# Kernel optimization log

Hardware: AMD Instinct MI355X
Metric: run time of the kernel (lower is better)

Reference implementation:

```python
import jax, jax.numpy as jnp
import numpy as np

H = 16
DH = 64  # n_state // n_head = 1024 // 16
EPS = 1e-6


def phi(x):
    return jax.nn.silu(x) + 1.0


def setup_inputs() -> dict:
    key = jax.random.key(0)
    ks = jax.random.split(key, 9)
    B, C, Tq, Tk = 8, 1024, 1500, 1500
    s = 1.0 / np.sqrt(C).astype(np.float32)
    return {
        "x": jax.random.normal(ks[0], (B, C, Tq, 1), jnp.float32),
        "xa": jax.random.normal(ks[1], (B, C, Tk, 1), jnp.float32),
        "Wq": jax.random.normal(ks[2], (C, C), jnp.float32) * s,
        "bq": jax.random.normal(ks[3], (C,), jnp.float32) * s,
        "Wk": jax.random.normal(ks[4], (C, C), jnp.float32) * s,
        "Wv": jax.random.normal(ks[5], (C, C), jnp.float32) * s,
        "bv": jax.random.normal(ks[6], (C,), jnp.float32) * s,
        "Wo": jax.random.normal(ks[7], (C, C), jnp.float32) * s,
        "bo": jax.random.normal(ks[8], (C,), jnp.float32) * s,
    }


def reference(x, xa, Wq, bq, Wk, Wv, bv, Wo, bo):
    # x: (B,C,Tq,1), xa: (B,C,Tk,1). 1x1 conv2d == matmul over channel dim.
    xq = x[..., 0]   # (B,C,Tq)
    xk = xa[..., 0]  # (B,C,Tk)
    q = jnp.einsum('oc,bct->bot', Wq, xq) + bq[None, :, None]
    k = jnp.einsum('oc,bct->bot', Wk, xk)  # key has no bias
    v = jnp.einsum('oc,bct->bot', Wv, xk) + bv[None, :, None]

    B, C, Tq = q.shape
    Tk = k.shape[2]
    pq = phi(q).reshape(B, H, DH, Tq)
    pk = phi(k).reshape(B, H, DH, Tk)
    vv = v.reshape(B, H, DH, Tk)

    k_sum = pk.sum(axis=3)            # (B,H,Dh) : sum_t phi(k)
    kv_sum = (pk * vv).sum(axis=3)    # (B,H,Dh) : diagonal phi(k)*v sum (as in source)
    den = jnp.einsum('bhdt,bhd->bht', pq, k_sum) + EPS  # (B,H,Tq)

    out = pq * kv_sum[..., None] / den[:, :, None, :]   # (B,H,Dh,Tq)
    out = out.reshape(B, C, Tq) / jnp.sqrt(jnp.asarray(DH, out.dtype))
    y = jnp.einsum('oc,bct->bot', Wo, out) + bo[None, :, None]
    return y[..., None]  # (B,C,Tq,1)
```

## Files before the change

kernel.cpp:

```cpp
#include <hip/hip_runtime.h>

typedef __attribute__((ext_vector_type(4))) float  f32x4;
typedef __attribute__((ext_vector_type(4))) float  float4v;
typedef __attribute__((ext_vector_type(8))) short  short8;
typedef __attribute__((ext_vector_type(4))) short  short4v;

#define TQ 1500
#define TP 1536
#define CC 1024
#define EPS 1e-6f

#define XT_OFF    ((size_t)0)
#define XAT_OFF   ((size_t)25165824)
#define OUT_OFF   ((size_t)50331648)
#define WB_OFF    ((size_t)75497472)
#define KSUM_OFF  ((size_t)83886080)
#define KVSUM_OFF ((size_t)83918848)

#define VMCNT4() asm volatile("s_waitcnt vmcnt(4)" ::: "memory")
#define VMCNT2() asm volatile("s_waitcnt vmcnt(2)" ::: "memory")
#define VMCNT0() asm volatile("s_waitcnt vmcnt(0)" ::: "memory")
#define LGKM0()  asm volatile("s_waitcnt lgkmcnt(0)" ::: "memory")
#define SBAR()   __builtin_amdgcn_s_barrier()
#define SCHED0() __builtin_amdgcn_sched_barrier(0)

__device__ __forceinline__ float bf2f(short s) {
    union { unsigned u; float f; } v; v.u = ((unsigned)(unsigned short)s) << 16; return v.f;
}
__device__ __forceinline__ short f2bf(float f) {
    union { float f; unsigned u; } v; v.f = f;
    unsigned r = (v.u + 0x7FFFu + ((v.u >> 16) & 1u)) >> 16;
    return (short)r;
}
__device__ __forceinline__ float phi_f(float x) {
    return x / (1.f + __expf(-x)) + 1.f;
}
__device__ __forceinline__ void gl_lds16(const void* g, void* l) {
    __builtin_amdgcn_global_load_lds((const __attribute__((address_space(1))) void*)g,
                                     (__attribute__((address_space(3))) void*)l, 16, 0, 0);
}


__global__ __launch_bounds__(256)
void conv_w_kernel(const float* __restrict__ w0, const float* __restrict__ w1,
                   const float* __restrict__ w2, const float* __restrict__ w3,
                   short* __restrict__ o0, short* __restrict__ o1,
                   short* __restrict__ o2, short* __restrict__ o3)
{
    const int i = (blockIdx.x * 256 + threadIdx.x) * 4;
    float4v a = *(const float4v*)(w0 + i);
    float4v b = *(const float4v*)(w1 + i);
    float4v c = *(const float4v*)(w2 + i);
    float4v d = *(const float4v*)(w3 + i);
    short4v ra, rb, rc, rd;
#pragma unroll
    for (int j = 0; j < 4; ++j) {
        ra[j] = f2bf(a[j]); rb[j] = f2bf(b[j]); rc[j] = f2bf(c[j]); rd[j] = f2bf(d[j]);
    }
    *(short4v*)(o0 + i) = ra;
    *(short4v*)(o1 + i) = rb;
    *(short4v*)(o2 + i) = rc;
    *(short4v*)(o3 + i) = rd;
}

__global__ __launch_bounds__(256)
void xpose_kernel(const float* __restrict__ x, const float* __restrict__ xa,
                  short* __restrict__ xT, short* __restrict__ xaT)
{
    __shared__ float tile[64][65];
    const int z  = blockIdx.z;
    const int b  = z & 7;
    const float* src = (z < 8) ? x : xa;
    short* dst       = (z < 8) ? xT : xaT;
    const int c0 = blockIdx.y * 64;
    const int t0 = blockIdx.x * 64;
    const int tl = threadIdx.x & 63;
    const int q  = threadIdx.x >> 6;
    const int t  = t0 + tl;
#pragma unroll
    for (int i = 0; i < 16; ++i) {
        const int cl = q * 16 + i;
        float v = 0.f;
        if (t < TQ) v = src[((size_t)b * CC + c0 + cl) * TQ + t];
        tile[cl][tl] = v;
    }
    __syncthreads();
#pragma unroll
    for (int i = 0; i < 16; ++i) {
        const int t2 = q * 16 + i;
        dst[((size_t)b * TP + t0 + t2) * CC + c0 + tl] = f2bf(tile[tl][t2]);
    }
}


__global__ __launch_bounds__(512, 4)
void gemm_q_out_kernel(const short* __restrict__ xT, const short* __restrict__ Wqb,
                       const float* __restrict__ bq, const float* __restrict__ ksum,
                       const float* __restrict__ kvsum, short* __restrict__ outT)
{
    __shared__ short lds[4][8192];
    const int f    = blockIdx.x;
    const int L    = (f & 7) * 96 + (f >> 3);
    const int nt   = L % 8;
    const int mrow = L / 8;
    const int b    = mrow / 12;
    const int tid  = threadIdx.x;
    const int wave = tid >> 6, lane = tid & 63;
    const int wr = wave >> 1;
    const int wc = wave & 1;
    const int rl = lane & 15;
    const int q4 = lane >> 4;
    const int rg = (q4 ^ ((rl >> 1) & 3)) << 3;
    const int rgrp = q4;

    const int srow = tid >> 2;
    const int skc  = ((tid & 3) ^ ((srow >> 1) & 3)) << 3;
    const short* aSrc = xT  + (size_t)(mrow * 128 + srow) * CC + skc;
    const short* bSrc = Wqb + (size_t)(nt   * 128 + srow) * CC + skc;
    const int dstOff = wave * 512;

    const int aoff0 = (wr * 32 + rl) * 32 + rg;
    const int boff0 = 4096 + (wc * 64 + rl) * 32 + rg;

    f32x4 acc[2][4] = {};

#pragma unroll
    for (int k0 = 0; k0 < 3; ++k0) {
        gl_lds16(aSrc + k0 * 32, &lds[k0][dstOff]);
        gl_lds16(bSrc + k0 * 32, &lds[k0][4096 + dstOff]);
    }
    VMCNT4(); SBAR();

#pragma unroll 1
    for (int kt = 0; kt < 32; ++kt) {
        if (kt < 29) {
            const int pn = (kt + 3) & 3;
            gl_lds16(aSrc + (kt + 3) * 32, &lds[pn][dstOff]);
            gl_lds16(bSrc + (kt + 3) * 32, &lds[pn][4096 + dstOff]);
        }
        const int p = kt & 3;
        const short* ba = &lds[p][aoff0];
        const short* bb = &lds[p][boff0];
        short8 ra[2], rb[4];
        ra[0] = *(const short8*)(ba);
        ra[1] = *(const short8*)(ba + 512);
        rb[0] = *(const short8*)(bb);
        rb[1] = *(const short8*)(bb + 512);
        rb[2] = *(const short8*)(bb + 1024);
        rb[3] = *(const short8*)(bb + 1536);
        LGKM0(); SCHED0();
        __builtin_amdgcn_s_setprio(1);
#pragma unroll
        for (int i = 0; i < 2; ++i)
#pragma unroll
            for (int j = 0; j < 4; ++j)
                acc[i][j] = __builtin_amdgcn_mfma_f32_16x16x32_bf16(ra[i], rb[j], acc[i][j], 0, 0, 0);
        __builtin_amdgcn_s_setprio(0);
        if (kt < 29)       { VMCNT4(); }
        else if (kt == 29) { VMCNT2(); }
        else if (kt == 30) { VMCNT0(); }
        if (kt < 31) SBAR();
    }

    float bias[4], ks[4], kv[4];
#pragma unroll
    for (int j = 0; j < 4; ++j) {
        const int c = nt * 128 + wc * 64 + j * 16 + rl;
        bias[j] = bq[c];
        ks[j]   = ksum[b * CC + c];
        kv[j]   = kvsum[b * CC + c];
    }
#pragma unroll
    for (int i = 0; i < 2; ++i)
#pragma unroll
        for (int j = 0; j < 4; ++j)
#pragma unroll
            for (int r = 0; r < 4; ++r)
                acc[i][j][r] = phi_f(acc[i][j][r] + bias[j]);
#pragma unroll
    for (int i = 0; i < 2; ++i) {
#pragma unroll
        for (int r = 0; r < 4; ++r) {
            float d = acc[i][0][r] * ks[0] + acc[i][1][r] * ks[1]
                    + acc[i][2][r] * ks[2] + acc[i][3][r] * ks[3];
            d += __shfl_xor(d, 1); d += __shfl_xor(d, 2);
            d += __shfl_xor(d, 4); d += __shfl_xor(d, 8);
            const float inv = 0.125f / (d + EPS);
            const int trow = mrow * 128 + wr * 32 + i * 16 + rgrp * 4 + r;
#pragma unroll
            for (int j = 0; j < 4; ++j) {
                const int c = nt * 128 + wc * 64 + j * 16 + rl;
                outT[(size_t)trow * CC + c] = f2bf(acc[i][j][r] * kv[j] * inv);
            }
        }
    }
}

__global__ __launch_bounds__(512, 4)
void gemm_kv_kernel(const short* __restrict__ xaT, const short* __restrict__ Wkb,
                    const short* __restrict__ Wvb, const float* __restrict__ bv,
                    float* __restrict__ ksum, float* __restrict__ kvsum)
{
    __shared__ short lds[4][8192];
    const int f    = blockIdx.x;
    const int L    = (f & 7) * 192 + (f >> 3);
    const int cb   = L % 16;
    const int mrow = L / 16;
    const int b    = mrow / 12;
    const int tid  = threadIdx.x;
    const int wave = tid >> 6, lane = tid & 63;
    const int wr = wave >> 1;
    const int wc = wave & 1;
    const int rl = lane & 15;
    const int q4 = lane >> 4;
    const int rg = (q4 ^ ((rl >> 1) & 3)) << 3;
    const int rgrp = q4;

    const int srow = tid >> 2;
    const int skc  = ((tid & 3) ^ ((srow >> 1) & 3)) << 3;
    const short* aSrc = xaT + (size_t)(mrow * 128 + srow) * CC + skc;
    const short* bSrc = (srow < 64)
        ? Wkb + (size_t)(cb * 64 + srow) * CC + skc
        : Wvb + (size_t)(cb * 64 + srow - 64) * CC + skc;
    const int dstOff = wave * 512;

    const int aoff0 = (wr * 32 + rl) * 32 + rg;
    const int boffK = 4096 + (wc * 32 + rl) * 32 + rg;
    const int boffV = boffK + 2048;

    f32x4 acc[2][4] = {};

#pragma unroll
    for (int k0 = 0; k0 < 3; ++k0) {
        gl_lds16(aSrc + k0 * 32, &lds[k0][dstOff]);
        gl_lds16(bSrc + k0 * 32, &lds[k0][4096 + dstOff]);
    }
    VMCNT4(); SBAR();

#pragma unroll 1
    for (int kt = 0; kt < 32; ++kt) {
        if (kt < 29) {
            const int pn = (kt + 3) & 3;
            gl_lds16(aSrc + (kt + 3) * 32, &lds[pn][dstOff]);
            gl_lds16(bSrc + (kt + 3) * 32, &lds[pn][4096 + dstOff]);
        }
        const int p = kt & 3;
        const short* ba = &lds[p][aoff0];
        short8 ra[2], rb[4];
        ra[0] = *(const short8*)(ba);
        ra[1] = *(const short8*)(ba + 512);
        rb[0] = *(const short8*)(&lds[p][boffK]);
        rb[1] = *(const short8*)(&lds[p][boffK + 512]);
        rb[2] = *(const short8*)(&lds[p][boffV]);
        rb[3] = *(const short8*)(&lds[p][boffV + 512]);
        LGKM0(); SCHED0();
        __builtin_amdgcn_s_setprio(1);
#pragma unroll
        for (int i = 0; i < 2; ++i)
#pragma unroll
            for (int j = 0; j < 4; ++j)
                acc[i][j] = __builtin_amdgcn_mfma_f32_16x16x32_bf16(ra[i], rb[j], acc[i][j], 0, 0, 0);
        __builtin_amdgcn_s_setprio(0);
        if (kt < 29)       { VMCNT4(); }
        else if (kt == 29) { VMCNT2(); }
        else if (kt == 30) { VMCNT0(); }
        if (kt < 31) SBAR();
    }

    const int tbase = (mrow % 12) * 128 + wr * 32 + rgrp * 4;
#pragma unroll
    for (int jj = 0; jj < 2; ++jj) {
        const int c = cb * 64 + wc * 32 + jj * 16 + rl;
        const float bvc = bv[c];
        float sk = 0.f, skv = 0.f;
#pragma unroll
        for (int i = 0; i < 2; ++i) {
#pragma unroll
            for (int r = 0; r < 4; ++r) {
                if (tbase + i * 16 + r < TQ) {
                    float pk = phi_f(acc[i][jj][r]);
                    float vv = acc[i][jj + 2][r] + bvc;
                    sk  += pk;
                    skv += pk * vv;
                }
            }
        }
        sk  += __shfl_xor(sk, 16);  sk  += __shfl_xor(sk, 32);
        skv += __shfl_xor(skv, 16); skv += __shfl_xor(skv, 32);
        if (rgrp == 0) {
            atomicAdd(&ksum[b * CC + c], sk);
            atomicAdd(&kvsum[b * CC + c], skv);
        }
    }
}

__global__ __launch_bounds__(512, 4)
void gemm_o_kernel(const short* __restrict__ Wob, const short* __restrict__ outT,
                   const float* __restrict__ bo, float* __restrict__ y)
{
    __shared__ short lds[4][8192];
    const int f    = blockIdx.x;
    const int L    = (f & 7) * 96 + (f >> 3);
    const int ct   = L % 8;
    const int rest = L / 8;
    const int b    = rest / 12;
    const int tt   = rest % 12;
    const int tid  = threadIdx.x;
    const int wave = tid >> 6, lane = tid & 63;
    const int wr = wave >> 1;
    const int wc = wave & 1;
    const int rl = lane & 15;
    const int q4 = lane >> 4;
    const int rg = (q4 ^ ((rl >> 1) & 3)) << 3;
    const int rgrp = q4;

    const int srow = tid >> 2;
    const int skc  = ((tid & 3) ^ ((srow >> 1) & 3)) << 3;
    const short* aSrc = Wob  + (size_t)(ct * 128 + srow) * CC + skc;
    const short* bSrc = outT + (size_t)(rest * 128 + srow) * CC + skc;
    const int dstOff = wave * 512;

    const int aoff0 = (wr * 32 + rl) * 32 + rg;
    const int boff0 = 4096 + (wc * 64 + rl) * 32 + rg;

    f32x4 acc[2][4] = {};

#pragma unroll
    for (int k0 = 0; k0 < 3; ++k0) {
        gl_lds16(aSrc + k0 * 32, &lds[k0][dstOff]);
        gl_lds16(bSrc + k0 * 32, &lds[k0][4096 + dstOff]);
    }
    VMCNT4(); SBAR();

#pragma unroll 1
    for (int kt = 0; kt < 32; ++kt) {
        if (kt < 29) {
            const int pn = (kt + 3) & 3;
            gl_lds16(aSrc + (kt + 3) * 32, &lds[pn][dstOff]);
            gl_lds16(bSrc + (kt + 3) * 32, &lds[pn][4096 + dstOff]);
        }
        const int p = kt & 3;
        const short* ba = &lds[p][aoff0];
        const short* bb = &lds[p][boff0];
        short8 ra[2], rb[4];
        ra[0] = *(const short8*)(ba);
        ra[1] = *(const short8*)(ba + 512);
        rb[0] = *(const short8*)(bb);
        rb[1] = *(const short8*)(bb + 512);
        rb[2] = *(const short8*)(bb + 1024);
        rb[3] = *(const short8*)(bb + 1536);
        LGKM0(); SCHED0();
        __builtin_amdgcn_s_setprio(1);
#pragma unroll
        for (int i = 0; i < 2; ++i)
#pragma unroll
            for (int j = 0; j < 4; ++j)
                acc[i][j] = __builtin_amdgcn_mfma_f32_16x16x32_bf16(ra[i], rb[j], acc[i][j], 0, 0, 0);
        __builtin_amdgcn_s_setprio(0);
        if (kt < 29)       { VMCNT4(); }
        else if (kt == 29) { VMCNT2(); }
        else if (kt == 30) { VMCNT0(); }
        if (kt < 31) SBAR();
    }

#pragma unroll
    for (int j = 0; j < 4; ++j) {
        const int t = tt * 128 + wc * 64 + j * 16 + rl;
        if (t >= TQ) continue;
#pragma unroll
        for (int i = 0; i < 2; ++i) {
            const int cbase = ct * 128 + wr * 32 + i * 16 + rgrp * 4;
#pragma unroll
            for (int r = 0; r < 4; ++r) {
                const int c = cbase + r;
                y[((size_t)b * CC + c) * TQ + t] = acc[i][j][r] + bo[c];
            }
        }
    }
}

extern "C" void kernel_launch(void* const* d_in, const int* in_sizes, int n_in,
                              void* d_out, int out_size, void* d_ws, size_t ws_size,
                              hipStream_t stream)
{
    (void)in_sizes; (void)n_in; (void)out_size; (void)ws_size;
    const float* x  = (const float*)d_in[0];
    const float* xa = (const float*)d_in[1];
    const float* Wq = (const float*)d_in[2];
    const float* bq = (const float*)d_in[3];
    const float* Wk = (const float*)d_in[4];
    const float* Wv = (const float*)d_in[5];
    const float* bv = (const float*)d_in[6];
    const float* Wo = (const float*)d_in[7];
    const float* bo = (const float*)d_in[8];
    float* y = (float*)d_out;
    char* ws = (char*)d_ws;

    short* xT    = (short*)(ws + XT_OFF);
    short* xaT   = (short*)(ws + XAT_OFF);
    short* outT  = (short*)(ws + OUT_OFF);
    short* Wqb   = (short*)(ws + WB_OFF);
    short* Wkb   = Wqb + (size_t)CC * CC;
    short* Wvb   = Wkb + (size_t)CC * CC;
    short* Wob   = Wvb + (size_t)CC * CC;
    float* ksum  = (float*)(ws + KSUM_OFF);
    float* kvsum = (float*)(ws + KVSUM_OFF);

    conv_w_kernel<<<dim3(CC * CC / 4 / 256), 256, 0, stream>>>(Wq, Wk, Wv, Wo, Wqb, Wkb, Wvb, Wob);
    xpose_kernel<<<dim3(TP / 64, CC / 64, 16), 256, 0, stream>>>(x, xa, xT, xaT);
    hipMemsetAsync(ws + KSUM_OFF, 0, 65536, stream);

    gemm_kv_kernel<<<dim3(1536), 512, 0, stream>>>(xaT, Wkb, Wvb, bv, ksum, kvsum);
    gemm_q_out_kernel<<<dim3(768), 512, 0, stream>>>(xT, Wqb, bq, ksum, kvsum, outT);
    gemm_o_kernel<<<dim3(768), 512, 0, stream>>>(Wob, outT, bo, y);
}
```

Baseline: 321.3 us.

## Use 4-wave blocks with 64x64 warp tiles and 3-stage LDS ring in GEMMs

All three GEMM kernels go from 8 waves per 128x128 tile to 4 waves, each wave now computing a 64x64 sub-tile (4x4 MFMA accumulators instead of 2x4). This doubles per-wave register reuse of LDS fragments and halves LDS reads per MFMA. The LDS ring shrinks from 4 to 3 stages, with prefetch distance 2, which reduces LDS footprint and so can raise occupancy. The costs are more accumulator registers per thread, fewer waves to hide latency, and a shallower prefetch pipeline.

```diff
diff --git a/kernel.cpp b/kernel.cpp
--- a/kernel.cpp
+++ b/kernel.cpp
@@ -18,7 +18,6 @@
 #define KVSUM_OFF ((size_t)83918848)
 
 #define VMCNT4() asm volatile("s_waitcnt vmcnt(4)" ::: "memory")
-#define VMCNT2() asm volatile("s_waitcnt vmcnt(2)" ::: "memory")
 #define VMCNT0() asm volatile("s_waitcnt vmcnt(0)" ::: "memory")
 #define LGKM0()  asm volatile("s_waitcnt lgkmcnt(0)" ::: "memory")
 #define SBAR()   __builtin_amdgcn_s_barrier()
@@ -93,12 +92,12 @@
 }
 
 
-__global__ __launch_bounds__(512, 4)
+__global__ __launch_bounds__(256, 4)
 void gemm_q_out_kernel(const short* __restrict__ xT, const short* __restrict__ Wqb,
                        const float* __restrict__ bq, const float* __restrict__ ksum,
                        const float* __restrict__ kvsum, short* __restrict__ outT)
 {
-    __shared__ short lds[4][8192];
+    __shared__ short lds[3][8192];
     const int f    = blockIdx.x;
     const int L    = (f & 7) * 96 + (f >> 3);
     const int nt   = L % 8;
@@ -111,55 +110,57 @@
     const int rl = lane & 15;
     const int q4 = lane >> 4;
     const int rg = (q4 ^ ((rl >> 1) & 3)) << 3;
-    const int rgrp = q4;
-
-    const int srow = tid >> 2;
-    const int skc  = ((tid & 3) ^ ((srow >> 1) & 3)) << 3;
-    const short* aSrc = xT  + (size_t)(mrow * 128 + srow) * CC + skc;
-    const short* bSrc = Wqb + (size_t)(nt   * 128 + srow) * CC + skc;
-    const int dstOff = wave * 512;
-
-    const int aoff0 = (wr * 32 + rl) * 32 + rg;
+
+    const int lrow = lane >> 2;
+    const int kc   = ((lane & 3) ^ ((lrow >> 1) & 3)) << 3;
+    const int row0 = wave * 32 + lrow;
+    const short* aP0 = xT  + (size_t)(mrow * 128 + row0) * CC + kc;
+    const short* aP1 = aP0 + 16 * CC;
+    const short* bP0 = Wqb + (size_t)(nt * 128 + row0) * CC + kc;
+    const short* bP1 = bP0 + 16 * CC;
+    const int aD0 = wave * 1024, aD1 = aD0 + 512;
+    const int bD0 = 4096 + aD0,  bD1 = bD0 + 512;
+
+    const int aoff0 = (wr * 64 + rl) * 32 + rg;
     const int boff0 = 4096 + (wc * 64 + rl) * 32 + rg;
 
-    f32x4 acc[2][4] = {};
-
-#pragma unroll
-    for (int k0 = 0; k0 < 3; ++k0) {
-        gl_lds16(aSrc + k0 * 32, &lds[k0][dstOff]);
-        gl_lds16(bSrc + k0 * 32, &lds[k0][4096 + dstOff]);
+    f32x4 acc[4][4] = {};
+
+#pragma unroll
+    for (int s = 0; s < 2; ++s) {
+        gl_lds16(aP0, &lds[s][aD0]); gl_lds16(aP1, &lds[s][aD1]);
+        gl_lds16(bP0, &lds[s][bD0]); gl_lds16(bP1, &lds[s][bD1]);
+        aP0 += 32; aP1 += 32; bP0 += 32; bP1 += 32;
     }
     VMCNT4(); SBAR();
 
+    int cur = 0;
 #pragma unroll 1
     for (int kt = 0; kt < 32; ++kt) {
-        if (kt < 29) {
-            const int pn = (kt + 3) & 3;
-            gl_lds16(aSrc + (kt + 3) * 32, &lds[pn][dstOff]);
-            gl_lds16(bSrc + (kt + 3) * 32, &lds[pn][4096 + dstOff]);
-        }
-        const int p = kt & 3;
-        const short* ba = &lds[p][aoff0];
-        const short* bb = &lds[p][boff0];
-        short8 ra[2], rb[4];
-        ra[0] = *(const short8*)(ba);
-        ra[1] = *(const short8*)(ba + 512);
-        rb[0] = *(const short8*)(bb);
-        rb[1] = *(const short8*)(bb + 512);
-        rb[2] = *(const short8*)(bb + 1024);
-        rb[3] = *(const short8*)(bb + 1536);
+        if (kt <= 29) {
+            const int pn = (cur == 0) ? 2 : cur - 1;
+            gl_lds16(aP0, &lds[pn][aD0]); gl_lds16(aP1, &lds[pn][aD1]);
+            gl_lds16(bP0, &lds[pn][bD0]); gl_lds16(bP1, &lds[pn][bD1]);
+            aP0 += 32; aP1 += 32; bP0 += 32; bP1 += 32;
+        }
+        short8 ra[4], rb[4];
+#pragma unroll
+        for (int i = 0; i < 4; ++i) {
+            ra[i] = *(const short8*)&lds[cur][aoff0 + i * 512];
+            rb[i] = *(const short8*)&lds[cur][boff0 + i * 512];
+        }
         LGKM0(); SCHED0();
         __builtin_amdgcn_s_setprio(1);
 #pragma unroll
-        for (int i = 0; i < 2; ++i)
+        for (int i = 0; i < 4; ++i)
 #pragma unroll
             for (int j = 0; j < 4; ++j)
                 acc[i][j] = __builtin_amdgcn_mfma_f32_16x16x32_bf16(ra[i], rb[j], acc[i][j], 0, 0, 0);
         __builtin_amdgcn_s_setprio(0);
-        if (kt < 29)       { VMCNT4(); }
-        else if (kt == 29) { VMCNT2(); }
+        if (kt <= 29)      { VMCNT4(); }
         else if (kt == 30) { VMCNT0(); }
         if (kt < 31) SBAR();
+        cur = (cur == 2) ? 0 : cur + 1;
     }
 
     float bias[4], ks[4], kv[4];
@@ -171,14 +172,14 @@
         kv[j]   = kvsum[b * CC + c];
     }
 #pragma unroll
-    for (int i = 0; i < 2; ++i)
+    for (int i = 0; i < 4; ++i)
 #pragma unroll
         for (int j = 0; j < 4; ++j)
 #pragma unroll
             for (int r = 0; r < 4; ++r)
                 acc[i][j][r] = phi_f(acc[i][j][r] + bias[j]);
 #pragma unroll
-    for (int i = 0; i < 2; ++i) {
+    for (int i = 0; i < 4; ++i) {
 #pragma unroll
         for (int r = 0; r < 4; ++r) {
             float d = acc[i][0][r] * ks[0] + acc[i][1][r] * ks[1]
@@ -186,7 +187,7 @@
             d += __shfl_xor(d, 1); d += __shfl_xor(d, 2);
             d += __shfl_xor(d, 4); d += __shfl_xor(d, 8);
             const float inv = 0.125f / (d + EPS);
-            const int trow = mrow * 128 + wr * 32 + i * 16 + rgrp * 4 + r;
+            const int trow = mrow * 128 + wr * 64 + i * 16 + q4 * 4 + r;
 #pragma unroll
             for (int j = 0; j < 4; ++j) {
                 const int c = nt * 128 + wc * 64 + j * 16 + rl;
@@ -196,12 +197,12 @@
     }
 }
 
-__global__ __launch_bounds__(512, 4)
+__global__ __launch_bounds__(256, 4)
 void gemm_kv_kernel(const short* __restrict__ xaT, const short* __restrict__ Wkb,
                     const short* __restrict__ Wvb, const float* __restrict__ bv,
                     float* __restrict__ ksum, float* __restrict__ kvsum)
 {
-    __shared__ short lds[4][8192];
+    __shared__ short lds[3][8192];
     const int f    = blockIdx.x;
     const int L    = (f & 7) * 192 + (f >> 3);
     const int cb   = L % 16;
@@ -214,70 +215,77 @@
     const int rl = lane & 15;
     const int q4 = lane >> 4;
     const int rg = (q4 ^ ((rl >> 1) & 3)) << 3;
-    const int rgrp = q4;
-
-    const int srow = tid >> 2;
-    const int skc  = ((tid & 3) ^ ((srow >> 1) & 3)) << 3;
-    const short* aSrc = xaT + (size_t)(mrow * 128 + srow) * CC + skc;
-    const short* bSrc = (srow < 64)
-        ? Wkb + (size_t)(cb * 64 + srow) * CC + skc
-        : Wvb + (size_t)(cb * 64 + srow - 64) * CC + skc;
-    const int dstOff = wave * 512;
-
-    const int aoff0 = (wr * 32 + rl) * 32 + rg;
+
+    const int lrow = lane >> 2;
+    const int kc   = ((lane & 3) ^ ((lrow >> 1) & 3)) << 3;
+    const int row0 = wave * 32 + lrow;
+    const short* aP0 = xaT + (size_t)(mrow * 128 + row0) * CC + kc;
+    const short* aP1 = aP0 + 16 * CC;
+    const short* bPanel = (wave < 2)
+        ? Wkb + (size_t)cb * 64 * CC
+        : Wvb + (size_t)cb * 64 * CC - (size_t)64 * CC;
+    const short* bP0 = bPanel + (size_t)row0 * CC + kc;
+    const short* bP1 = bP0 + 16 * CC;
+    const int aD0 = wave * 1024, aD1 = aD0 + 512;
+    const int bD0 = 4096 + aD0,  bD1 = bD0 + 512;
+
+    const int aoff0 = (wr * 64 + rl) * 32 + rg;
     const int boffK = 4096 + (wc * 32 + rl) * 32 + rg;
     const int boffV = boffK + 2048;
 
-    f32x4 acc[2][4] = {};
-
-#pragma unroll
-    for (int k0 = 0; k0 < 3; ++k0) {
-        gl_lds16(aSrc + k0 * 32, &lds[k0][dstOff]);
-        gl_lds16(bSrc + k0 * 32, &lds[k0][4096 + dstOff]);
+    f32x4 acc[4][4] = {};
+
+#pragma unroll
+    for (int s = 0; s < 2; ++s) {
+        gl_lds16(aP0, &lds[s][aD0]); gl_lds16(aP1, &lds[s][aD1]);
+        gl_lds16(bP0, &lds[s][bD0]); gl_lds16(bP1, &lds[s][bD1]);
+        aP0 += 32; aP1 += 32; bP0 += 32; bP1 += 32;
     }
     VMCNT4(); SBAR();
 
+    int cur = 0;
 #pragma unroll 1
     for (int kt = 0; kt < 32; ++kt) {
-        if (kt < 29) {
-            const int pn = (kt + 3) & 3;
-            gl_lds16(aSrc + (kt + 3) * 32, &lds[pn][dstOff]);
-            gl_lds16(bSrc + (kt + 3) * 32, &lds[pn][4096 + dstOff]);
-        }
-        const int p = kt & 3;
-        const short* ba = &lds[p][aoff0];
-        short8 ra[2], rb[4];
-        ra[0] = *(const short8*)(ba);
-        ra[1] = *(const short8*)(ba + 512);
-        rb[0] = *(const short8*)(&lds[p][boffK]);
-        rb[1] = *(const short8*)(&lds[p][boffK + 512]);
-        rb[2] = *(const short8*)(&lds[p][boffV]);
-        rb[3] = *(const short8*)(&lds[p][boffV + 512]);
+        if (kt <= 29) {
+            const int pn = (cur == 0) ? 2 : cur - 1;
+            gl_lds16(aP0, &lds[pn][aD0]); gl_lds16(aP1, &lds[pn][aD1]);
+            gl_lds16(bP0, &lds[pn][bD0]); gl_lds16(bP1, &lds[pn][bD1]);
+            aP0 += 32; aP1 += 32; bP0 += 32; bP1 += 32;
+        }
+        short8 ra[4], rb[4];
+#pragma unroll
+        for (int i = 0; i < 4; ++i)
+            ra[i] = *(const short8*)&lds[cur][aoff0 + i * 512];
+#pragma unroll
+        for (int j = 0; j < 2; ++j) {
+            rb[j]     = *(const short8*)&lds[cur][boffK + j * 512];
+            rb[j + 2] = *(const short8*)&lds[cur][boffV + j * 512];
+        }
         LGKM0(); SCHED0();
         __builtin_amdgcn_s_setprio(1);
 #pragma unroll
-        for (int i = 0; i < 2; ++i)
+        for (int i = 0; i < 4; ++i)
 #pragma unroll
             for (int j = 0; j < 4; ++j)
                 acc[i][j] = __builtin_amdgcn_mfma_f32_16x16x32_bf16(ra[i], rb[j], acc[i][j], 0, 0, 0);
         __builtin_amdgcn_s_setprio(0);
-        if (kt < 29)       { VMCNT4(); }
-        else if (kt == 29) { VMCNT2(); }
+        if (kt <= 29)      { VMCNT4(); }
         else if (kt == 30) { VMCNT0(); }
         if (kt < 31) SBAR();
-    }
-
-    const int tbase = (mrow % 12) * 128 + wr * 32 + rgrp * 4;
+        cur = (cur == 2) ? 0 : cur + 1;
+    }
+
+    const int tq0 = (mrow % 12) * 128 + wr * 64 + q4 * 4;
 #pragma unroll
     for (int jj = 0; jj < 2; ++jj) {
         const int c = cb * 64 + wc * 32 + jj * 16 + rl;
         const float bvc = bv[c];
         float sk = 0.f, skv = 0.f;
 #pragma unroll
-        for (int i = 0; i < 2; ++i) {
+        for (int i = 0; i < 4; ++i) {
 #pragma unroll
             for (int r = 0; r < 4; ++r) {
-                if (tbase + i * 16 + r < TQ) {
+                if (tq0 + i * 16 + r < TQ) {
                     float pk = phi_f(acc[i][jj][r]);
                     float vv = acc[i][jj + 2][r] + bvc;
                     sk  += pk;
@@ -287,18 +295,18 @@
         }
         sk  += __shfl_xor(sk, 16);  sk  += __shfl_xor(sk, 32);
         skv += __shfl_xor(skv, 16); skv += __shfl_xor(skv, 32);
-        if (rgrp == 0) {
+        if (q4 == 0) {
             atomicAdd(&ksum[b * CC + c], sk);
             atomicAdd(&kvsum[b * CC + c], skv);
         }
     }
 }
 
-__global__ __launch_bounds__(512, 4)
+__global__ __launch_bounds__(256, 4)
 void gemm_o_kernel(const short* __restrict__ Wob, const short* __restrict__ outT,
                    const float* __restrict__ bo, float* __restrict__ y)
 {
-    __shared__ short lds[4][8192];
+    __shared__ short lds[3][8192];
     const int f    = blockIdx.x;
     const int L    = (f & 7) * 96 + (f >> 3);
     const int ct   = L % 8;
@@ -312,55 +320,57 @@
     const int rl = lane & 15;
     const int q4 = lane >> 4;
     const int rg = (q4 ^ ((rl >> 1) & 3)) << 3;
-    const int rgrp = q4;
-
-    const int srow = tid >> 2;
-    const int skc  = ((tid & 3) ^ ((srow >> 1) & 3)) << 3;
-    const short* aSrc = Wob  + (size_t)(ct * 128 + srow) * CC + skc;
-    const short* bSrc = outT + (size_t)(rest * 128 + srow) * CC + skc;
-    const int dstOff = wave * 512;
-
-    const int aoff0 = (wr * 32 + rl) * 32 + rg;
+
+    const int lrow = lane >> 2;
+    const int kc   = ((lane & 3) ^ ((lrow >> 1) & 3)) << 3;
+    const int row0 = wave * 32 + lrow;
+    const short* aP0 = Wob  + (size_t)(ct * 128 + row0) * CC + kc;
+    const short* aP1 = aP0 + 16 * CC;
+    const short* bP0 = outT + (size_t)(rest * 128 + row0) * CC + kc;
+    const short* bP1 = bP0 + 16 * CC;
+    const int aD0 = wave * 1024, aD1 = aD0 + 512;
+    const int bD0 = 4096 + aD0,  bD1 = bD0 + 512;
+
+    const int aoff0 = (wr * 64 + rl) * 32 + rg;
     const int boff0 = 4096 + (wc * 64 + rl) * 32 + rg;
 
-    f32x4 acc[2][4] = {};
-
-#pragma unroll
-    for (int k0 = 0; k0 < 3; ++k0) {
-        gl_lds16(aSrc + k0 * 32, &lds[k0][dstOff]);
-        gl_lds16(bSrc + k0 * 32, &lds[k0][4096 + dstOff]);
+    f32x4 acc[4][4] = {};
+
+#pragma unroll
+    for (int s = 0; s < 2; ++s) {
+        gl_lds16(aP0, &lds[s][aD0]); gl_lds16(aP1, &lds[s][aD1]);
+        gl_lds16(bP0, &lds[s][bD0]); gl_lds16(bP1, &lds[s][bD1]);
+        aP0 += 32; aP1 += 32; bP0 += 32; bP1 += 32;
     }
     VMCNT4(); SBAR();
 
+    int cur = 0;
 #pragma unroll 1
     for (int kt = 0; kt < 32; ++kt) {
-        if (kt < 29) {
-            const int pn = (kt + 3) & 3;
-            gl_lds16(aSrc + (kt + 3) * 32, &lds[pn][dstOff]);
-            gl_lds16(bSrc + (kt + 3) * 32, &lds[pn][4096 + dstOff]);
-        }
-        const int p = kt & 3;
-        const short* ba = &lds[p][aoff0];
-        const short* bb = &lds[p][boff0];
-        short8 ra[2], rb[4];
-        ra[0] = *(const short8*)(ba);
-        ra[1] = *(const short8*)(ba + 512);
-        rb[0] = *(const short8*)(bb);
-        rb[1] = *(const short8*)(bb + 512);
-        rb[2] = *(const short8*)(bb + 1024);
-        rb[3] = *(const short8*)(bb + 1536);
+        if (kt <= 29) {
+            const int pn = (cur == 0) ? 2 : cur - 1;
+            gl_lds16(aP0, &lds[pn][aD0]); gl_lds16(aP1, &lds[pn][aD1]);
+            gl_lds16(bP0, &lds[pn][bD0]); gl_lds16(bP1, &lds[pn][bD1]);
+            aP0 += 32; aP1 += 32; bP0 += 32; bP1 += 32;
+        }
+        short8 ra[4], rb[4];
+#pragma unroll
+        for (int i = 0; i < 4; ++i) {
+            ra[i] = *(const short8*)&lds[cur][aoff0 + i * 512];
+            rb[i] = *(const short8*)&lds[cur][boff0 + i * 512];
+        }
         LGKM0(); SCHED0();
         __builtin_amdgcn_s_setprio(1);
 #pragma unroll
-        for (int i = 0; i < 2; ++i)
+        for (int i = 0; i < 4; ++i)
 #pragma unroll
             for (int j = 0; j < 4; ++j)
                 acc[i][j] = __builtin_amdgcn_mfma_f32_16x16x32_bf16(ra[i], rb[j], acc[i][j], 0, 0, 0);
         __builtin_amdgcn_s_setprio(0);
-        if (kt < 29)       { VMCNT4(); }
-        else if (kt == 29) { VMCNT2(); }
+        if (kt <= 29)      { VMCNT4(); }
         else if (kt == 30) { VMCNT0(); }
         if (kt < 31) SBAR();
+        cur = (cur == 2) ? 0 : cur + 1;
     }
 
 #pragma unroll
@@ -368,8 +378,8 @@
         const int t = tt * 128 + wc * 64 + j * 16 + rl;
         if (t >= TQ) continue;
 #pragma unroll
-        for (int i = 0; i < 2; ++i) {
-            const int cbase = ct * 128 + wr * 32 + i * 16 + rgrp * 4;
+        for (int i = 0; i < 4; ++i) {
+            const int cbase = ct * 128 + wr * 64 + i * 16 + q4 * 4;
 #pragma unroll
             for (int r = 0; r < 4; ++r) {
                 const int c = cbase + r;
@@ -410,7 +420,7 @@
     xpose_kernel<<<dim3(TP / 64, CC / 64, 16), 256, 0, stream>>>(x, xa, xT, xaT);
     hipMemsetAsync(ws + KSUM_OFF, 0, 65536, stream);
 
-    gemm_kv_kernel<<<dim3(1536), 512, 0, stream>>>(xaT, Wkb, Wvb, bv, ksum, kvsum);
-    gemm_q_out_kernel<<<dim3(768), 512, 0, stream>>>(xT, Wqb, bq, ksum, kvsum, outT);
-    gemm_o_kernel<<<dim3(768), 512, 0, stream>>>(Wob, outT, bo, y);
-}
+    gemm_kv_kernel<<<dim3(1536), 256, 0, stream>>>(xaT, Wkb, Wvb, bv, ksum, kvsum);
+    gemm_q_out_kernel<<<dim3(768), 256, 0, stream>>>(xT, Wqb, bq, ksum, kvsum, outT);
+    gemm_o_kernel<<<dim3(768), 256, 0, stream>>>(Wob, outT, bo, y);
+}
```

Measured after the change: 324.8 us. About the same (+1.1%).
